# Kernel optimization log

Hardware: AMD Instinct MI355X
Metric: run time of the kernel (lower is better)

Reference implementation:

```python
import jax, jax.numpy as jnp
import numpy as np

HEADS = 8
HD = 64            # hidden_channels per head
WIN = 16 * 16      # prod(window_size)
SCALE = HD ** -0.5


def setup_inputs() -> dict:
    key = jax.random.key(0)
    ks = jax.random.split(key, 8)
    B, C, H, W = 2, 128, 128, 128
    ROT = 32
    x = jax.random.normal(ks[0], (B, C, H, W), jnp.float32)
    skip = jax.random.normal(ks[1], (B, C, H, W), jnp.float32)
    ang = jax.random.uniform(ks[2], (H, W, ROT), jnp.float32) * 6.2831853
    sin = jnp.sin(ang)
    cos = jnp.cos(ang)
    Wq = jax.random.normal(ks[3], (HEADS * HD, C), jnp.float32) * 0.05
    Wkv = jax.random.normal(ks[4], (2 * HEADS * HD, C), jnp.float32) * 0.05
    Wout = jax.random.normal(ks[5], (C, HEADS * HD), jnp.float32) * 0.05
    return {"x": x, "skip": skip, "sin": sin, "cos": cos,
            "Wq": Wq, "Wkv": Wkv, "Wout": Wout}


def _rotate_half_pairs(t):
    # torch: reshape(..., -1, 2); stack([-even, odd], -1); reshape back
    t2 = t.reshape(t.shape[:-1] + (-1, 2))
    return jnp.stack([-t2[..., 0], t2[..., 1]], axis=-1).reshape(t.shape)


def reference(x, skip, sin, cos, Wq, Wkv, Wout):
    B, C, H, W = x.shape
    rot = sin.shape[-1]

    # 1x1 convs (no bias) as channel contractions
    q = jnp.einsum('oc,bchw->bohw', Wq, x)                 # [B, heads*hd, H, W]
    kv_input = jnp.concatenate([x, skip], axis=0)          # [2B, C, H, W]
    kv = jnp.einsum('oc,bchw->bohw', Wkv, kv_input)        # [2B, 2*heads*hd, H, W]
    k, v = jnp.split(kv, 2, axis=1)

    # faithful raw reshape (memory reinterpretation, as in the source)
    def rs(t):
        return t.reshape(HEADS * t.shape[0], H, W, -1)
    q, k, v = rs(q), rs(k), rs(v)

    # inline RoPE (faithful, including the `k = k + cos` quirk of the source)
    q_r, q_pass = q[..., :rot], q[..., rot:]
    k_r, k_pass = k[..., :rot], k[..., rot:]
    q_r = q_r * cos + _rotate_half_pairs(q_r) * sin
    k_r = k_r + cos + _rotate_half_pairs(k_r) * sin
    q = jnp.concatenate([q_r, q_pass], axis=-1)
    k = jnp.concatenate([k_r, k_pass], axis=-1)

    def towin(t):
        n = int(np.prod(t.shape[:-1])) // WIN
        return t.reshape(n, WIN, t.shape[-1])
    q, k, v = towin(q), towin(k), towin(v)

    # skip-KV concat: halve window-batch, double window length
    k = k.reshape(k.shape[0] // 2, 2 * WIN, k.shape[2])
    v = v.reshape(v.shape[0] // 2, 2 * WIN, v.shape[2])

    sim = jnp.einsum('bid,bjd->bij', q, k) * SCALE
    attn = jax.nn.softmax(sim, axis=-1)
    out = jnp.einsum('bij,bjd->bid', attn, v)

    out = out.reshape(B, HEADS * out.shape[2], H, W)       # faithful raw reshape
    out = jnp.einsum('oc,bchw->bohw', Wout, out)           # [B, C, H, W]
    return out
```

## Files before the change

### kernel.cpp

```cpp
#include <hip/hip_runtime.h>
#include <hip/hip_bf16.h>


typedef unsigned short u16;
using bfrag = __attribute__((ext_vector_type(8))) short;
using ffrag = __attribute__((ext_vector_type(4))) float;
using s4v   = __attribute__((ext_vector_type(4))) short;
using u32x4 = __attribute__((ext_vector_type(4))) unsigned int;

#define MFMA16(a, b, c) __builtin_amdgcn_mfma_f32_16x16x32_bf16((a), (b), (c), 0, 0, 0)
#define QSCALE 0.1803368801111204f

__device__ __forceinline__ u16 f2bf(float f) {
    __hip_bfloat16 h = __float2bfloat16(f);
    u16 u;
    __builtin_memcpy(&u, &h, 2);
    return u;
}

__device__ __forceinline__ int sw(int p) { return (p ^ (p >> 3)) & 15; }

__global__ __launch_bounds__(256) void k_prep(
    const float* __restrict__ Wq, const float* __restrict__ Wkv,
    const float* __restrict__ Wout, u16* __restrict__ WB, u16* __restrict__ WoutB)
{
    int i8 = (blockIdx.x * 256 + threadIdx.x) * 8;
    const float* src;
    u16* dst;
    if (i8 < 65536)       { src = Wq + i8;            dst = WB + i8; }
    else if (i8 < 196608) { src = Wkv + (i8 - 65536); dst = WB + i8; }
    else                  { src = Wout + (i8 - 196608); dst = WoutB + (i8 - 196608); }
    float4 a = *(const float4*)src;
    float4 b = *(const float4*)(src + 4);
    u16 tmp[8];
    tmp[0] = f2bf(a.x); tmp[1] = f2bf(a.y); tmp[2] = f2bf(a.z); tmp[3] = f2bf(a.w);
    tmp[4] = f2bf(b.x); tmp[5] = f2bf(b.y); tmp[6] = f2bf(b.z); tmp[7] = f2bf(b.w);
    *(uint4*)dst = *(uint4*)tmp;
}

__global__ __launch_bounds__(256) void k_cast(
    const float* __restrict__ x, const float* __restrict__ skip,
    u16* __restrict__ xb)
{
    __shared__ float LT[128 * 65];
    const int t = threadIdx.x;
    const int pos0 = blockIdx.x * 64;
    const int p = blockIdx.y;
    const float* src = (p < 2) ? (x + (size_t)p * 2097152)
                               : (skip + (size_t)(p - 2) * 2097152);
    u16* dst = xb + (size_t)p * 2097152;

#pragma unroll
    for (int it = 0; it < 8; ++it) {
        int idx = it * 256 + t;
        int c = idx >> 4, p4 = (idx & 15) * 4;
        float4 v = *(const float4*)(src + (size_t)c * 16384 + pos0 + p4);
        LT[c * 65 + p4 + 0] = v.x;
        LT[c * 65 + p4 + 1] = v.y;
        LT[c * 65 + p4 + 2] = v.z;
        LT[c * 65 + p4 + 3] = v.w;
    }
    __syncthreads();

#pragma unroll
    for (int it = 0; it < 4; ++it) {
        int g = it * 256 + t;
        int pos_l = g >> 4, chunk = g & 15;
        u16 tmp[8];
#pragma unroll
        for (int j = 0; j < 8; ++j)
            tmp[j] = f2bf(LT[(chunk * 8 + j) * 65 + pos_l]);
        *(uint4*)(dst + (size_t)(pos0 + pos_l) * 128 + chunk * 8) = *(uint4*)tmp;
    }
}

__global__ __launch_bounds__(256, 4) void k_proj(
    const u16* __restrict__ xb, const float* __restrict__ sinp,
    const float* __restrict__ cosp, const u16* __restrict__ WB,
    u16* __restrict__ qb, u16* __restrict__ kbuf, u16* __restrict__ vbuf)
{
    __shared__ u16 BT[64 * 128];
    __shared__ float2 SC2[64][33];
    const int t = threadIdx.x;
    const int pos0 = blockIdx.x * 64;
    const int tr = blockIdx.y;
    const int w = t >> 6, l = t & 63, lr = l & 15, lg = l >> 4;

    int WBrow, plane, mode;
    u16* dst;
    const bool contig = (tr >= 8);
    if (tr < 8) {
        int b = tr >> 2, o0 = (tr & 3) * 128;
        WBrow = o0; plane = b; mode = 1;
        dst = qb + (size_t)b * 8388608 + (size_t)o0 * 16384;
    } else {
        int t2 = tr - 8;
        int bkv = t2 >> 3, oo0 = (t2 & 7) * 128;
        WBrow = 512 + oo0; plane = bkv;
        if (oo0 < 512) {
            dst = kbuf + (size_t)bkv * 8388608 + (size_t)blockIdx.x * 32768 + (size_t)oo0 * 64;
            mode = 2;
        } else {
            dst = vbuf + (size_t)bkv * 8388608 + (size_t)blockIdx.x * 32768 + (size_t)(oo0 - 512) * 64;
            mode = 0;
        }
    }

    const u16* xsrc = xb + (size_t)plane * 2097152 + (size_t)pos0 * 128;
#pragma unroll
    for (int it = 0; it < 4; ++it) {
        int li = it * 256 + t;
        int row = li >> 4, chunk = li & 15;
        uint4 v = *(const uint4*)(xsrc + (size_t)row * 128 + chunk * 8);
        *(uint4*)&BT[row * 128 + ((chunk ^ sw(row)) << 3)] = v;
    }

    const int hh = pos0 >> 7;
    const int wwhi = blockIdx.x & 1;
    if (mode != 0) {
        const int hb = hh >> 6;
        const int ridx = (hh & 63) * 2 + wwhi;
#pragma unroll
        for (int e = 0; e < 2; ++e) {
            int g = e * 256 + t;
            int row = g >> 3;
            int q = g & 7;
            size_t base = ((size_t)(row * 2 + hb) * 128 + ridx) * 32 + q * 4;
            float4 sv4 = *(const float4*)(sinp + base);
            float4 cv4 = *(const float4*)(cosp + base);
            SC2[row][q * 4 + 0] = float2{sv4.x, cv4.x};
            SC2[row][q * 4 + 1] = float2{sv4.y, cv4.y};
            SC2[row][q * 4 + 2] = float2{sv4.z, cv4.z};
            SC2[row][q * 4 + 3] = float2{sv4.w, cv4.w};
        }
    }

    ffrag zf = {0.f, 0.f, 0.f, 0.f};
    ffrag acc[4][2];
#pragma unroll
    for (int mb = 0; mb < 4; ++mb)
#pragma unroll
        for (int nb = 0; nb < 2; ++nb) acc[mb][nb] = zf;

    __syncthreads();

#pragma unroll
    for (int kk = 0; kk < 4; ++kk) {
        bfrag A[4], B[2];
#pragma unroll
        for (int mb = 0; mb < 4; ++mb) {
            int pos_l = mb * 16 + lr;
            A[mb] = *(const bfrag*)&BT[pos_l * 128 + (((kk * 4 + lg) ^ sw(pos_l)) << 3)];
        }
#pragma unroll
        for (int nb = 0; nb < 2; ++nb)
            B[nb] = *(const bfrag*)(WB + (size_t)(WBrow + w * 32 + nb * 16 + lr) * 128 + kk * 32 + lg * 8);
#pragma unroll
        for (int mb = 0; mb < 4; ++mb)
#pragma unroll
            for (int nb = 0; nb < 2; ++nb)
                acc[mb][nb] = MFMA16(A[mb], B[nb], acc[mb][nb]);
    }

    __syncthreads();

#pragma unroll
    for (int mb = 0; mb < 4; ++mb) {
        const bool roped = (mode != 0) && (mb < 2);
#pragma unroll
        for (int nb = 0; nb < 2; ++nb) {
            int o_l = w * 32 + nb * 16 + lr;
            int p0 = mb * 16 + lg * 4;
            ffrag v4 = acc[mb][nb];
            if (roped) {
                const int ob63 = o_l & 63;
#pragma unroll
                for (int r = 0; r < 4; ++r) {
                    float2 sc = SC2[ob63][p0 + r];
                    float sg = (r & 1) ? sc.x : -sc.x;
                    v4[r] = (mode == 1) ? v4[r] * (sc.y + sg)
                                        : v4[r] * (1.f + sg) + sc.y;
                }
            }
            if (mode == 1) {
#pragma unroll
                for (int r = 0; r < 4; ++r) v4[r] *= QSCALE;
            }
            s4v pk;
            pk[0] = (short)f2bf(v4[0]); pk[1] = (short)f2bf(v4[1]);
            pk[2] = (short)f2bf(v4[2]); pk[3] = (short)f2bf(v4[3]);
            int slot = p0 >> 3;
            *(s4v*)&BT[o_l * 64 + ((slot ^ (o_l & 7)) << 3) + (p0 & 4)] = pk;
        }
    }

#pragma unroll
    for (int it = 0; it < 4; ++it) {
        int i = it * 64 + l;
        int row = w * 32 + (i >> 3);
        int slot = i & 7;
        u32x4 v = *(const u32x4*)&BT[row * 64 + ((slot ^ (row & 7)) << 3)];
        size_t goff = contig ? ((size_t)row * 64 + slot * 8)
                             : ((size_t)row * 16384 + pos0 + slot * 8);
        __builtin_nontemporal_store(v, (u32x4*)(dst + goff));
    }
}

__global__ __launch_bounds__(256) void k_attn(
    const u16* __restrict__ qb, const u16* __restrict__ kbuf,
    const u16* __restrict__ vbuf, u16* __restrict__ ob)
{
    __shared__ u16 Ks[64 * 64];
    __shared__ u16 Vt[64 * 64];
    __shared__ u16 Ps[4][64 * 40];

    const int bp = blockIdx.x;
    const int t = threadIdx.x, w = t >> 6, l = t & 63, lr = l & 15, lg = l >> 4;

    const u16* Qg = qb + (size_t)bp * 16384 + w * 4096;

    bfrag Qf[4][2];
#pragma unroll
    for (int rb = 0; rb < 4; ++rb)
#pragma unroll
        for (int dk = 0; dk < 2; ++dk)
            Qf[rb][dk] = *(const bfrag*)(Qg + (rb * 16 + lr) * 64 + dk * 32 + lg * 8);

    ffrag zf = {0.f, 0.f, 0.f, 0.f};
    ffrag Oacc[4][4];
#pragma unroll
    for (int rb = 0; rb < 4; ++rb)
#pragma unroll
        for (int sb = 0; sb < 4; ++sb) Oacc[rb][sb] = zf;
    float Lp[4] = {0.f, 0.f, 0.f, 0.f};

    const int tk = t & 127, sj = tk >> 1, half = tk & 1;
    const bool isK = (t < 128);
    const size_t kvoff = (size_t)(bp >> 8) * 8388608 + (size_t)(bp & 255) * 128;
    const u16* gsb = (isK ? kbuf : vbuf) + kvoff;
    #define KVOFF(c) ((size_t)(((c) & 3) * 64 + sj) * 32768 + (size_t)(((c) >> 2) * 64) + half * 32)

    uint4 r0 = *(const uint4*)(gsb + KVOFF(0));
    uint4 r1 = *(const uint4*)(gsb + KVOFF(0) + 8);
    uint4 r2 = *(const uint4*)(gsb + KVOFF(0) + 16);
    uint4 r3 = *(const uint4*)(gsb + KVOFF(0) + 24);

    for (int c = 0; c < 8; ++c) {
        __syncthreads();
        if (isK) {
            *(uint4*)&Ks[sj * 64 + (((half * 4 + 0) ^ (sj & 7)) << 3)] = r0;
            *(uint4*)&Ks[sj * 64 + (((half * 4 + 1) ^ (sj & 7)) << 3)] = r1;
            *(uint4*)&Ks[sj * 64 + (((half * 4 + 2) ^ (sj & 7)) << 3)] = r2;
            *(uint4*)&Ks[sj * 64 + (((half * 4 + 3) ^ (sj & 7)) << 3)] = r3;
        } else {
            u16 tmp[32];
            *(uint4*)&tmp[0] = r0;
            *(uint4*)&tmp[8] = r1;
            *(uint4*)&tmp[16] = r2;
            *(uint4*)&tmp[24] = r3;
            const int chunk = sj >> 3, jl = sj & 7;
#pragma unroll
            for (int e = 0; e < 32; ++e) {
                int d = half * 32 + e;
                int s = (d & 7) ^ ((d >> 3) & 7);
                Vt[d * 64 + ((chunk ^ s) << 3) + jl] = tmp[e];
            }
        }
        __syncthreads();
        if (c < 7) {
            r0 = *(const uint4*)(gsb + KVOFF(c + 1));
            r1 = *(const uint4*)(gsb + KVOFF(c + 1) + 8);
            r2 = *(const uint4*)(gsb + KVOFF(c + 1) + 16);
            r3 = *(const uint4*)(gsb + KVOFF(c + 1) + 24);
        }

#pragma unroll
        for (int jh = 0; jh < 2; ++jh) {
#pragma unroll
            for (int jtl = 0; jtl < 2; ++jtl) {
                const int jt = jh * 2 + jtl;
                bfrag Kf[2];
#pragma unroll
                for (int dk = 0; dk < 2; ++dk)
                    Kf[dk] = *(const bfrag*)&Ks[(jt * 16 + lr) * 64 + (((dk * 4 + lg) ^ (lr & 7)) << 3)];
#pragma unroll
                for (int rb = 0; rb < 4; ++rb) {
                    ffrag sf = zf;
                    __builtin_amdgcn_s_setprio(1);
                    sf = MFMA16(Kf[0], Qf[rb][0], sf);
                    sf = MFMA16(Kf[1], Qf[rb][1], sf);
                    __builtin_amdgcn_s_setprio(0);
                    float e0 = __builtin_amdgcn_exp2f(sf[0]);
                    float e1 = __builtin_amdgcn_exp2f(sf[1]);
                    float e2 = __builtin_amdgcn_exp2f(sf[2]);
                    float e3 = __builtin_amdgcn_exp2f(sf[3]);
                    Lp[rb] += (e0 + e1) + (e2 + e3);
                    s4v pk;
                    pk[0] = (short)f2bf(e0); pk[1] = (short)f2bf(e1);
                    pk[2] = (short)f2bf(e2); pk[3] = (short)f2bf(e3);
                    *(s4v*)&Ps[w][(rb * 16 + lr) * 40 + jtl * 16 + lg * 4] = pk;
                }
            }

            bfrag Vf[4];
#pragma unroll
            for (int sb = 0; sb < 4; ++sb) {
                int d = sb * 16 + lr;
                int s = (d & 7) ^ ((d >> 3) & 7);
                Vf[sb] = *(const bfrag*)&Vt[d * 64 + (((jh * 4 + lg) ^ s) << 3)];
            }
            __builtin_amdgcn_s_setprio(1);
#pragma unroll
            for (int rb = 0; rb < 4; ++rb) {
                bfrag Pf = *(const bfrag*)&Ps[w][(rb * 16 + lr) * 40 + lg * 8];
#pragma unroll
                for (int sb = 0; sb < 4; ++sb)
                    Oacc[rb][sb] = MFMA16(Vf[sb], Pf, Oacc[rb][sb]);
            }
            __builtin_amdgcn_s_setprio(0);
        }
    }
    #undef KVOFF

    u16* og = ob + (size_t)bp * 16384 + w * 4096;
#pragma unroll
    for (int rb = 0; rb < 4; ++rb) {
        float v = Lp[rb];
        v += __shfl_xor(v, 16);
        v += __shfl_xor(v, 32);
        float inv = 1.f / v;
#pragma unroll
        for (int sb = 0; sb < 4; ++sb) {
            s4v pk;
#pragma unroll
            for (int r = 0; r < 4; ++r)
                pk[r] = (short)f2bf(Oacc[rb][sb][r] * inv);
            *(s4v*)(og + (rb * 16 + lr) * 64 + sb * 16 + lg * 4) = pk;
        }
    }
}

__global__ __launch_bounds__(256) void k_out(
    const u16* __restrict__ ob, const u16* __restrict__ WoutB,
    float* __restrict__ out)
{
    __shared__ u16 OT[64 * 128];
    const int t = threadIdx.x, w = t >> 6, l = t & 63, lr = l & 15, lg = l >> 4;
    const int pos0 = blockIdx.x * 64;
    const int b = blockIdx.y;
    const u16* obp = ob + (size_t)b * 8388608;
    float* op = out + (size_t)b * 2097152;

    ffrag zf = {0.f, 0.f, 0.f, 0.f};
    ffrag acc[2][4];
#pragma unroll
    for (int rb = 0; rb < 2; ++rb)
#pragma unroll
        for (int nb = 0; nb < 4; ++nb) acc[rb][nb] = zf;

    for (int kc = 0; kc < 4; ++kc) {
        __syncthreads();
#pragma unroll
        for (int it = 0; it < 4; ++it) {
            int g = it * 256 + t;
            int cl = g >> 3, pk = g & 7;
            uint4 v = *(const uint4*)(obp + (size_t)(kc * 128 + cl) * 16384 + pos0 + pk * 8);
            u16 tmp[8];
            *(uint4*)tmp = v;
#pragma unroll
            for (int e = 0; e < 8; ++e) {
                int pos_l = pk * 8 + e;
                OT[pos_l * 128 + (((cl >> 3) ^ sw(pos_l)) << 3) + (cl & 7)] = tmp[e];
            }
        }
        __syncthreads();

#pragma unroll
        for (int kk = 0; kk < 4; ++kk) {
            bfrag Af[2];
#pragma unroll
            for (int rb = 0; rb < 2; ++rb)
                Af[rb] = *(const bfrag*)(WoutB + (size_t)(w * 32 + rb * 16 + lr) * 512 + kc * 128 + kk * 32 + lg * 8);
#pragma unroll
            for (int nb = 0; nb < 4; ++nb) {
                int pos_l = nb * 16 + lr;
                bfrag B = *(const bfrag*)&OT[pos_l * 128 + (((kk * 4 + lg) ^ sw(pos_l)) << 3)];
#pragma unroll
                for (int rb = 0; rb < 2; ++rb)
                    acc[rb][nb] = MFMA16(Af[rb], B, acc[rb][nb]);
            }
        }
    }

#pragma unroll
    for (int rb = 0; rb < 2; ++rb)
#pragma unroll
        for (int nb = 0; nb < 4; ++nb)
#pragma unroll
            for (int r = 0; r < 4; ++r)
                __builtin_nontemporal_store(acc[rb][nb][r],
                    op + (size_t)(w * 32 + rb * 16 + lg * 4 + r) * 16384 + pos0 + nb * 16 + lr);
}

extern "C" void kernel_launch(void* const* d_in, const int* in_sizes, int n_in,
                              void* d_out, int out_size, void* d_ws, size_t ws_size,
                              hipStream_t stream) {
    const float* x    = (const float*)d_in[0];
    const float* skip = (const float*)d_in[1];
    const float* sinp = (const float*)d_in[2];
    const float* cosp = (const float*)d_in[3];
    const float* Wq   = (const float*)d_in[4];
    const float* Wkv  = (const float*)d_in[5];
    const float* Wout = (const float*)d_in[6];
    float* out = (float*)d_out;

    u16* qb    = (u16*)d_ws;
    u16* kbp   = qb + (size_t)16777216;
    u16* vbp   = kbp + (size_t)33554432;
    u16* xbp   = vbp + (size_t)33554432;
    u16* WBp   = xbp + (size_t)8388608;
    u16* WoutB = WBp + (size_t)196608;

    hipLaunchKernelGGL(k_prep, dim3(128), dim3(256), 0, stream,
                       Wq, Wkv, Wout, WBp, WoutB);
    hipLaunchKernelGGL(k_cast, dim3(256, 4), dim3(256), 0, stream,
                       x, skip, xbp);
    hipLaunchKernelGGL(k_proj, dim3(256, 40), dim3(256), 0, stream,
                       xbp, sinp, cosp, WBp, qb, kbp, vbp);
    hipLaunchKernelGGL(k_attn, dim3(1024), dim3(256), 0, stream,
                       qb, kbp, vbp, qb );
    hipLaunchKernelGGL(k_out, dim3(256, 2), dim3(256), 0, stream,
                       qb, WoutB, out);
}
```

Measured before the change: 149.1 us.

## Double-buffer K/V shared memory tiles in attention kernel to cut barriers

```diff
diff --git a/kernel.cpp b/kernel.cpp
--- a/kernel.cpp
+++ b/kernel.cpp
@@ -210,8 +210,8 @@
     const u16* __restrict__ qb, const u16* __restrict__ kbuf,
     const u16* __restrict__ vbuf, u16* __restrict__ ob)
 {
-    __shared__ u16 Ks[64 * 64];
-    __shared__ u16 Vt[64 * 64];
+    __shared__ u16 Ks[2][64 * 64];
+    __shared__ u16 Vt[2][64 * 64];
     __shared__ u16 Ps[4][64 * 40];
 
     const int bp = blockIdx.x;
@@ -239,39 +239,62 @@
     const size_t kvoff = (size_t)(bp >> 8) * 8388608 + (size_t)(bp & 255) * 128;
     const u16* gsb = (isK ? kbuf : vbuf) + kvoff;
     #define KVOFF(c) ((size_t)(((c) & 3) * 64 + sj) * 32768 + (size_t)(((c) >> 2) * 64) + half * 32)
-
-    uint4 r0 = *(const uint4*)(gsb + KVOFF(0));
-    uint4 r1 = *(const uint4*)(gsb + KVOFF(0) + 8);
-    uint4 r2 = *(const uint4*)(gsb + KVOFF(0) + 16);
-    uint4 r3 = *(const uint4*)(gsb + KVOFF(0) + 24);
+    const int chv = sj >> 3, jlv = sj & 7;
+
+    uint4 r0, r1, r2, r3;
+
+    r0 = *(const uint4*)(gsb + KVOFF(0));
+    r1 = *(const uint4*)(gsb + KVOFF(0) + 8);
+    r2 = *(const uint4*)(gsb + KVOFF(0) + 16);
+    r3 = *(const uint4*)(gsb + KVOFF(0) + 24);
+    if (isK) {
+        *(uint4*)&Ks[0][sj * 64 + (((half * 4 + 0) ^ (sj & 7)) << 3)] = r0;
+        *(uint4*)&Ks[0][sj * 64 + (((half * 4 + 1) ^ (sj & 7)) << 3)] = r1;
+        *(uint4*)&Ks[0][sj * 64 + (((half * 4 + 2) ^ (sj & 7)) << 3)] = r2;
+        *(uint4*)&Ks[0][sj * 64 + (((half * 4 + 3) ^ (sj & 7)) << 3)] = r3;
+    } else {
+        u16 tmp[32];
+        *(uint4*)&tmp[0] = r0;  *(uint4*)&tmp[8] = r1;
+        *(uint4*)&tmp[16] = r2; *(uint4*)&tmp[24] = r3;
+#pragma unroll
+        for (int e = 0; e < 32; ++e) {
+            int d = half * 32 + e;
+            int s = (d & 7) ^ ((d >> 3) & 7);
+            Vt[0][d * 64 + ((chv ^ s) << 3) + jlv] = tmp[e];
+        }
+    }
+    r0 = *(const uint4*)(gsb + KVOFF(1));
+    r1 = *(const uint4*)(gsb + KVOFF(1) + 8);
+    r2 = *(const uint4*)(gsb + KVOFF(1) + 16);
+    r3 = *(const uint4*)(gsb + KVOFF(1) + 24);
+    __syncthreads();
 
     for (int c = 0; c < 8; ++c) {
-        __syncthreads();
-        if (isK) {
-            *(uint4*)&Ks[sj * 64 + (((half * 4 + 0) ^ (sj & 7)) << 3)] = r0;
-            *(uint4*)&Ks[sj * 64 + (((half * 4 + 1) ^ (sj & 7)) << 3)] = r1;
-            *(uint4*)&Ks[sj * 64 + (((half * 4 + 2) ^ (sj & 7)) << 3)] = r2;
-            *(uint4*)&Ks[sj * 64 + (((half * 4 + 3) ^ (sj & 7)) << 3)] = r3;
-        } else {
-            u16 tmp[32];
-            *(uint4*)&tmp[0] = r0;
-            *(uint4*)&tmp[8] = r1;
-            *(uint4*)&tmp[16] = r2;
-            *(uint4*)&tmp[24] = r3;
-            const int chunk = sj >> 3, jl = sj & 7;
-#pragma unroll
-            for (int e = 0; e < 32; ++e) {
-                int d = half * 32 + e;
-                int s = (d & 7) ^ ((d >> 3) & 7);
-                Vt[d * 64 + ((chunk ^ s) << 3) + jl] = tmp[e];
-            }
-        }
-        __syncthreads();
+        const int cur = c & 1, nxt = cur ^ 1;
+
         if (c < 7) {
-            r0 = *(const uint4*)(gsb + KVOFF(c + 1));
-            r1 = *(const uint4*)(gsb + KVOFF(c + 1) + 8);
-            r2 = *(const uint4*)(gsb + KVOFF(c + 1) + 16);
-            r3 = *(const uint4*)(gsb + KVOFF(c + 1) + 24);
+            if (isK) {
+                *(uint4*)&Ks[nxt][sj * 64 + (((half * 4 + 0) ^ (sj & 7)) << 3)] = r0;
+                *(uint4*)&Ks[nxt][sj * 64 + (((half * 4 + 1) ^ (sj & 7)) << 3)] = r1;
+                *(uint4*)&Ks[nxt][sj * 64 + (((half * 4 + 2) ^ (sj & 7)) << 3)] = r2;
+                *(uint4*)&Ks[nxt][sj * 64 + (((half * 4 + 3) ^ (sj & 7)) << 3)] = r3;
+            } else {
+                u16 tmp[32];
+                *(uint4*)&tmp[0] = r0;  *(uint4*)&tmp[8] = r1;
+                *(uint4*)&tmp[16] = r2; *(uint4*)&tmp[24] = r3;
+#pragma unroll
+                for (int e = 0; e < 32; ++e) {
+                    int d = half * 32 + e;
+                    int s = (d & 7) ^ ((d >> 3) & 7);
+                    Vt[nxt][d * 64 + ((chv ^ s) << 3) + jlv] = tmp[e];
+                }
+            }
+        }
+        if (c < 6) {
+            r0 = *(const uint4*)(gsb + KVOFF(c + 2));
+            r1 = *(const uint4*)(gsb + KVOFF(c + 2) + 8);
+            r2 = *(const uint4*)(gsb + KVOFF(c + 2) + 16);
+            r3 = *(const uint4*)(gsb + KVOFF(c + 2) + 24);
         }
 
 #pragma unroll
@@ -282,7 +305,7 @@
                 bfrag Kf[2];
 #pragma unroll
                 for (int dk = 0; dk < 2; ++dk)
-                    Kf[dk] = *(const bfrag*)&Ks[(jt * 16 + lr) * 64 + (((dk * 4 + lg) ^ (lr & 7)) << 3)];
+                    Kf[dk] = *(const bfrag*)&Ks[cur][(jt * 16 + lr) * 64 + (((dk * 4 + lg) ^ (lr & 7)) << 3)];
 #pragma unroll
                 for (int rb = 0; rb < 4; ++rb) {
                     ffrag sf = zf;
@@ -307,7 +330,7 @@
             for (int sb = 0; sb < 4; ++sb) {
                 int d = sb * 16 + lr;
                 int s = (d & 7) ^ ((d >> 3) & 7);
-                Vf[sb] = *(const bfrag*)&Vt[d * 64 + (((jh * 4 + lg) ^ s) << 3)];
+                Vf[sb] = *(const bfrag*)&Vt[cur][d * 64 + (((jh * 4 + lg) ^ s) << 3)];
             }
             __builtin_amdgcn_s_setprio(1);
 #pragma unroll
@@ -319,6 +342,8 @@
             }
             __builtin_amdgcn_s_setprio(0);
         }
+
+        __syncthreads();
     }
     #undef KVOFF
 
```

After: 169.3 us. 13.6% more time.
